# Kernel tuning notes

Hardware: AMD Instinct MI355X
Metric: run time of the kernel (lower is better)

Reference implementation:

```python
import jax, jax.numpy as jnp
import numpy as np

N = 100000   # nodes
E = 1600000  # edges
F_IN = 256   # input features
H = 64       # hidden
C = 40       # classes


def setup_inputs() -> dict:
    key = jax.random.key(0)
    k = jax.random.split(key, 5)
    x = jax.random.normal(k[0], (N, F_IN), dtype=jnp.float32)
    edge_index = jax.random.randint(k[1], (2, E), 0, N, dtype=jnp.int64)
    edge_attr = jax.random.uniform(k[2], (E,), dtype=jnp.float32)
    # GCNConv params (glorot-ish scale), biases zero like reset_parameters
    W1 = jax.random.normal(k[3], (F_IN, H), dtype=jnp.float32) * (1.0 / np.sqrt(F_IN))
    b1 = jnp.zeros((H,), dtype=jnp.float32)
    W2 = jax.random.normal(k[4], (H, C), dtype=jnp.float32) * (1.0 / np.sqrt(H))
    b2 = jnp.zeros((C,), dtype=jnp.float32)
    return {"x": x, "edge_index": edge_index, "edge_attr": edge_attr,
            "W1": W1, "b1": b1, "W2": W2, "b2": b2}


def _gcn_conv(x, W, b, src, dst, norm):
    h = x @ W                                   # [N, out]
    msg = h[src] * norm[:, None]                # gather + edge scale [E+N, out]
    out = jax.ops.segment_sum(msg, dst, num_segments=N)
    return out + b


def reference(x, edge_index, edge_attr, W1, b1, W2, b2):
    # gcn_norm: add self-loops (weight 1), symmetric D^-1/2 A D^-1/2
    loop = jnp.arange(N, dtype=edge_index.dtype)
    src = jnp.concatenate([edge_index[0], loop])
    dst = jnp.concatenate([edge_index[1], loop])
    w = jnp.concatenate([edge_attr, jnp.ones((N,), dtype=edge_attr.dtype)])
    deg = jax.ops.segment_sum(w, dst, num_segments=N)
    dinv = jnp.where(deg > 0, jax.lax.rsqrt(jnp.maximum(deg, 1e-30)), 0.0)
    norm = dinv[src] * w * dinv[dst]

    h = _gcn_conv(x, W1, b1, src, dst, norm)
    h = jax.nn.relu(h)                          # dropout is identity in eval mode
    h = _gcn_conv(h, W2, b2, src, dst, norm)
    return jax.nn.log_softmax(h, axis=1)
```

## Files before the change

kernel.cpp:

```cpp
#include <hip/hip_runtime.h>
#include <math.h>

#define NN   100000
#define NE   1600000
#define FIN  256
#define HID  64
#define NC   40
#define NBKT 391
#define EPB  6250
#define CAP  4608

typedef __attribute__((ext_vector_type(8))) short short8;
typedef __attribute__((ext_vector_type(4))) float float4v;

static __device__ __forceinline__ short f2bf(float f) {
    unsigned u = __float_as_uint(f);
    u += 0x7FFFu + ((u >> 16) & 1u);
    return (short)(u >> 16);
}
static __device__ __forceinline__ float bf2f(unsigned short b) {
    return __uint_as_float((unsigned)b << 16);
}

__global__ __launch_bounds__(256) void w1cvt_k(const float* __restrict__ W1,
                                               short* __restrict__ w1t) {
    int t = blockIdx.x * 256 + threadIdx.x;
    int k = t >> 6, n = t & 63;
    w1t[n * FIN + k] = f2bf(W1[k * HID + n]);
}

__global__ __launch_bounds__(256) void phaseA_k(const int* __restrict__ src,
                                                const int* __restrict__ dst,
                                                const float* __restrict__ w,
                                                int* __restrict__ cursor,
                                                int2* __restrict__ bucketbuf) {
    __shared__ int  hist[NBKT];
    __shared__ int  sc[512];
    __shared__ int  loc_base[NBKT];
    __shared__ int  loc_cur[NBKT];
    __shared__ int  gb[NBKT];
    __shared__ int2 buf[EPB];
    const int t  = threadIdx.x;
    const int e0 = blockIdx.x * EPB;

    for (int i = t; i < NBKT; i += 256) hist[i] = 0;
    __syncthreads();
    for (int i = t; i < EPB; i += 256) atomicAdd(&hist[dst[e0 + i] >> 8], 1);
    __syncthreads();
    sc[t]       = (t       < NBKT) ? hist[t]       : 0;
    sc[t + 256] = (t + 256 < NBKT) ? hist[t + 256] : 0;
    __syncthreads();
    for (int off = 1; off < 512; off <<= 1) {
        int a0 = (t >= off) ? sc[t - off] : 0;
        int a1 = sc[t + 256 - off];
        __syncthreads();
        sc[t] += a0; sc[t + 256] += a1;
        __syncthreads();
    }
    for (int i = t; i < NBKT; i += 256) {
        int base = sc[i] - hist[i];
        loc_base[i] = base;
        loc_cur[i]  = base;
        gb[i] = atomicAdd(&cursor[i * 16], hist[i]);
    }
    __syncthreads();
    for (int i = t; i < EPB; i += 256) {
        int e = e0 + i;
        int d = dst[e];
        int b = d >> 8;
        int p = atomicAdd(&loc_cur[b], 1);
        buf[p] = make_int2(src[e] | ((d & 255) << 17), __float_as_int(w[e]));
    }
    __syncthreads();
    for (int b = t; b < NBKT; b += 256) {
        int lb = loc_base[b], n = hist[b];
        int2* dstp = bucketbuf + (size_t)b * CAP + gb[b];
        for (int i = 0; i < n; ++i) dstp[i] = buf[lb + i];
    }
}

__global__ __launch_bounds__(512) void scanB_k(const int* __restrict__ cursor,
                                               int* __restrict__ bucketbase,
                                               int* __restrict__ row_start) {
    __shared__ int tmp[512];
    int t = threadIdx.x;
    int v = (t < NBKT) ? cursor[t * 16] : 0;
    tmp[t] = v;
    __syncthreads();
    for (int off = 1; off < 512; off <<= 1) {
        int add = (t >= off) ? tmp[t - off] : 0;
        __syncthreads(); tmp[t] += add; __syncthreads();
    }
    if (t < NBKT) bucketbase[t] = tmp[t] - v;
    if (t == 0) { bucketbase[NBKT] = NE; row_start[NN] = NE; }
}

__global__ __launch_bounds__(256) void phaseB_k(const int* __restrict__ bucketbase,
                                                const int2* __restrict__ bucketbuf,
                                                int2* __restrict__ e8,
                                                int* __restrict__ row_start,
                                                float* __restrict__ dinv) {
    __shared__ int2 buf[CAP];
    __shared__ int2 buf2[CAP];
    __shared__ int  hist2[256];
    __shared__ int  tmp[256];
    __shared__ int  base2[257];
    __shared__ int  cur2[256];
    const int b = blockIdx.x, t = threadIdx.x;
    const int g0   = bucketbase[b];
    const int cntb = bucketbase[b + 1] - g0;
    const int n0   = b * 256;
    const int nnb  = (NN - n0 < 256) ? (NN - n0) : 256;

    hist2[t] = 0;
    __syncthreads();
    const int2* bb = bucketbuf + (size_t)b * CAP;
    for (int i = t; i < cntb; i += 256) {
        int2 kv = bb[i];
        buf[i] = kv;
        atomicAdd(&hist2[kv.x >> 17], 1);
    }
    __syncthreads();
    int v = hist2[t];
    tmp[t] = v;
    __syncthreads();
    for (int off = 1; off < 256; off <<= 1) {
        int add = (t >= off) ? tmp[t - off] : 0;
        __syncthreads(); tmp[t] += add; __syncthreads();
    }
    int excl = tmp[t] - v;
    base2[t] = excl;
    cur2[t]  = excl;
    if (t == 0) base2[256] = cntb;
    if (t < nnb) row_start[n0 + t] = g0 + excl;
    __syncthreads();
    for (int i = t; i < cntb; i += 256) {
        int2 kv = buf[i];
        int d = kv.x >> 17;
        int p = atomicAdd(&cur2[d], 1);
        buf2[p] = make_int2(kv.x & 0x1FFFF, kv.y);
    }
    __syncthreads();
    for (int i = t; i < cntb; i += 256) e8[g0 + i] = buf2[i];
    if (t < nnb) {
        float s = 0.f;
        int j1 = base2[t + 1];
        for (int j = base2[t]; j < j1; ++j) s += __int_as_float(buf2[j].y);
        dinv[n0 + t] = rsqrtf(1.0f + s);
    }
}

__global__ __launch_bounds__(256) void gemm1_mfma_k(const float* __restrict__ x,
                                                    const short* __restrict__ w1t,
                                                    const float* __restrict__ dinv,
                                                    unsigned short* __restrict__ h1) {
    const int wave = threadIdx.x >> 6;
    const int lane = threadIdx.x & 63;
    const int m    = lane & 15;
    const int quad = lane >> 4;
    const int r0   = blockIdx.x * 64 + wave * 16;
    const int row  = r0 + m;
    const int rcl  = (row < NN) ? row : (NN - 1);
    const float* xrow = x + (size_t)rcl * FIN + quad * 8;

    float4v acc0 = {0.f,0.f,0.f,0.f}, acc1 = acc0, acc2 = acc0, acc3 = acc0;

#pragma unroll
    for (int kc = 0; kc < 8; ++kc) {
        const int kof = kc * 32 + quad * 8;
        float4 xa = *(const float4*)(xrow + kc * 32);
        float4 xb = *(const float4*)(xrow + kc * 32 + 4);
        short8 a;
        a[0] = f2bf(xa.x); a[1] = f2bf(xa.y); a[2] = f2bf(xa.z); a[3] = f2bf(xa.w);
        a[4] = f2bf(xb.x); a[5] = f2bf(xb.y); a[6] = f2bf(xb.z); a[7] = f2bf(xb.w);
        short8 b0 = *(const short8*)(w1t + (0 * 16 + m) * FIN + kof);
        short8 b1 = *(const short8*)(w1t + (1 * 16 + m) * FIN + kof);
        short8 b2 = *(const short8*)(w1t + (2 * 16 + m) * FIN + kof);
        short8 b3 = *(const short8*)(w1t + (3 * 16 + m) * FIN + kof);
        acc0 = __builtin_amdgcn_mfma_f32_16x16x32_bf16(a, b0, acc0, 0, 0, 0);
        acc1 = __builtin_amdgcn_mfma_f32_16x16x32_bf16(a, b1, acc1, 0, 0, 0);
        acc2 = __builtin_amdgcn_mfma_f32_16x16x32_bf16(a, b2, acc2, 0, 0, 0);
        acc3 = __builtin_amdgcn_mfma_f32_16x16x32_bf16(a, b3, acc3, 0, 0, 0);
    }
#pragma unroll
    for (int r = 0; r < 4; ++r) {
        int rr = r0 + quad * 4 + r;
        if (rr < NN) {
            float dv = dinv[rr];
            unsigned short* hp = h1 + (size_t)rr * HID + m;
            hp[0]  = (unsigned short)f2bf(acc0[r] * dv);
            hp[16] = (unsigned short)f2bf(acc1[r] * dv);
            hp[32] = (unsigned short)f2bf(acc2[r] * dv);
            hp[48] = (unsigned short)f2bf(acc3[r] * dv);
        }
    }
}

__global__ __launch_bounds__(256) void gatherA_k(const int* __restrict__ row_start,
                                                 const int2* __restrict__ e8,
                                                 const float* __restrict__ dinv,
                                                 const unsigned short* __restrict__ h,
                                                 const float* __restrict__ b1,
                                                 unsigned short* __restrict__ Rp) {
    const int v    = blockIdx.x * 4 + (threadIdx.x >> 6);
    const int lane = threadIdx.x & 63;
    const int half = lane >> 5;
    const int fp2  = (lane & 31) << 1;
    const int i0 = row_start[v], i1 = row_start[v + 1];

    float a0 = 0.f, a1 = 0.f, c0 = 0.f, c1 = 0.f;
    int i = i0 + half;
    for (; i + 2 < i1; i += 4) {
        int2 ea = e8[i];
        int2 eb = e8[i + 2];
        unsigned pa = *(const unsigned*)(h + (size_t)ea.x * HID + fp2);
        unsigned pb = *(const unsigned*)(h + (size_t)eb.x * HID + fp2);
        float wa = __int_as_float(ea.y), wb = __int_as_float(eb.y);
        a0 = fmaf(__uint_as_float(pa << 16),          wa, a0);
        a1 = fmaf(__uint_as_float(pa & 0xFFFF0000u), wa, a1);
        c0 = fmaf(__uint_as_float(pb << 16),          wb, c0);
        c1 = fmaf(__uint_as_float(pb & 0xFFFF0000u), wb, c1);
    }
    if (i < i1) {
        int2 ea = e8[i];
        unsigned pa = *(const unsigned*)(h + (size_t)ea.x * HID + fp2);
        float wa = __int_as_float(ea.y);
        a0 = fmaf(__uint_as_float(pa << 16),          wa, a0);
        a1 = fmaf(__uint_as_float(pa & 0xFFFF0000u), wa, a1);
    }
    a0 += c0; a1 += c1;
    a0 += __shfl_xor(a0, 32);
    a1 += __shfl_xor(a1, 32);

    const float dv = dinv[v];
    unsigned ps = *(const unsigned*)(h + (size_t)v * HID + fp2);
    float r0 = dv * (a0 + __uint_as_float(ps << 16));
    float r1 = dv * (a1 + __uint_as_float(ps & 0xFFFF0000u));
    r0 = fmaxf(r0 + b1[fp2],     0.f);
    r1 = fmaxf(r1 + b1[fp2 + 1], 0.f);
    if (half == 0) {
        unsigned pk = (unsigned)(unsigned short)f2bf(dv * r0)
                    | ((unsigned)(unsigned short)f2bf(dv * r1) << 16);
        *(unsigned*)(Rp + (size_t)v * HID + fp2) = pk;
    }
}

__global__ __launch_bounds__(256) void gatherB_k(const int* __restrict__ row_start,
                                                 const int2* __restrict__ e8,
                                                 const float* __restrict__ dinv,
                                                 const unsigned short* __restrict__ Rp,
                                                 float* __restrict__ agg2) {
    const int v    = blockIdx.x * 4 + (threadIdx.x >> 6);
    const int lane = threadIdx.x & 63;
    const int half = lane >> 5;
    const int fp2  = (lane & 31) << 1;
    const int i0 = row_start[v], i1 = row_start[v + 1];

    float a0 = 0.f, a1 = 0.f, c0 = 0.f, c1 = 0.f;
    int i = i0 + half;
    for (; i + 2 < i1; i += 4) {
        int2 ea = e8[i];
        int2 eb = e8[i + 2];
        unsigned pa = *(const unsigned*)(Rp + (size_t)ea.x * HID + fp2);
        unsigned pb = *(const unsigned*)(Rp + (size_t)eb.x * HID + fp2);
        float wa = __int_as_float(ea.y), wb = __int_as_float(eb.y);
        a0 = fmaf(__uint_as_float(pa << 16),          wa, a0);
        a1 = fmaf(__uint_as_float(pa & 0xFFFF0000u), wa, a1);
        c0 = fmaf(__uint_as_float(pb << 16),          wb, c0);
        c1 = fmaf(__uint_as_float(pb & 0xFFFF0000u), wb, c1);
    }
    if (i < i1) {
        int2 ea = e8[i];
        unsigned pa = *(const unsigned*)(Rp + (size_t)ea.x * HID + fp2);
        float wa = __int_as_float(ea.y);
        a0 = fmaf(__uint_as_float(pa << 16),          wa, a0);
        a1 = fmaf(__uint_as_float(pa & 0xFFFF0000u), wa, a1);
    }
    a0 += c0; a1 += c1;
    a0 += __shfl_xor(a0, 32);
    a1 += __shfl_xor(a1, 32);

    const float dv = dinv[v];
    unsigned ps = *(const unsigned*)(Rp + (size_t)v * HID + fp2);
    float r0 = dv * (a0 + __uint_as_float(ps << 16));
    float r1 = dv * (a1 + __uint_as_float(ps & 0xFFFF0000u));
    if (half == 0)
        *(float2*)(agg2 + (size_t)v * HID + fp2) = make_float2(r0, r1);
}

__global__ __launch_bounds__(256) void gemm3_logsm_k(const float* __restrict__ agg2,
                                                     const float* __restrict__ W2,
                                                     const float* __restrict__ b2,
                                                     float* __restrict__ out) {
    __shared__ float w2s[HID * NC];
    __shared__ float b2s[NC];
    for (int i = threadIdx.x; i < HID * NC; i += 256) w2s[i] = W2[i];
    if (threadIdx.x < NC) b2s[threadIdx.x] = b2[threadIdx.x];
    __syncthreads();

    const int r = blockIdx.x * 256 + threadIdx.x;
    if (r >= NN) return;
    float acc[NC];
#pragma unroll
    for (int c = 0; c < NC; ++c) acc[c] = b2s[c];

    const float4* row4 = (const float4*)(agg2 + (size_t)r * HID);
    for (int kk = 0; kk < HID; kk += 4) {
        float4 v = row4[kk >> 2];
#pragma unroll
        for (int c = 0; c < NC; ++c) {
            acc[c] = fmaf(v.x, w2s[(kk + 0) * NC + c], acc[c]);
            acc[c] = fmaf(v.y, w2s[(kk + 1) * NC + c], acc[c]);
            acc[c] = fmaf(v.z, w2s[(kk + 2) * NC + c], acc[c]);
            acc[c] = fmaf(v.w, w2s[(kk + 3) * NC + c], acc[c]);
        }
    }
    float m = acc[0];
#pragma unroll
    for (int c = 1; c < NC; ++c) m = fmaxf(m, acc[c]);
    float s = 0.f;
#pragma unroll
    for (int c = 0; c < NC; ++c) s += __expf(acc[c] - m);
    float lg = m + __logf(s);
    float* outp = out + (size_t)r * NC;
#pragma unroll
    for (int c = 0; c < NC; c += 4)
        *(float4*)&outp[c] = make_float4(acc[c] - lg, acc[c+1] - lg, acc[c+2] - lg, acc[c+3] - lg);
}

extern "C" void kernel_launch(void* const* d_in, const int* in_sizes, int n_in,
                              void* d_out, int out_size, void* d_ws, size_t ws_size,
                              hipStream_t stream) {
    const float* x  = (const float*)d_in[0];
    const int*   ei = (const int*)d_in[1];
    const float* ea = (const float*)d_in[2];
    const float* W1 = (const float*)d_in[3];
    const float* b1 = (const float*)d_in[4];
    const float* W2 = (const float*)d_in[5];
    const float* b2 = (const float*)d_in[6];
    const int* src = ei;
    const int* dst = ei + NE;
    float* out = (float*)d_out;

    char* ws = (char*)d_ws;
    float* dinv       = (float*)(ws + 0);
    int*   row_start  = (int*)  (ws + 400000);
    int*   cursor     = (int*)  (ws + 800016);
    int*   bucketbase = (int*)  (ws + 825040);
    int2*  e8         = (int2*) (ws + 826608);
    unsigned short* h1 = (unsigned short*)(ws + 13626608);
    unsigned short* Rp = (unsigned short*)(ws + 26426608);
    float* agg2       = (float*)(ws + 39226608);
    short* w1t        = (short*)(ws + 64826608);
    int2*  bucketbuf  = (int2*)agg2;

    hipMemsetAsync(cursor, 0, 391 * 16 * sizeof(int), stream);

    w1cvt_k <<<64,   256, 0, stream>>>(W1, w1t);
    phaseA_k<<<256,  256, 0, stream>>>(src, dst, ea, cursor, bucketbuf);
    scanB_k <<<1,    512, 0, stream>>>(cursor, bucketbase, row_start);
    phaseB_k<<<NBKT, 256, 0, stream>>>(bucketbase, bucketbuf, e8, row_start, dinv);

    gemm1_mfma_k <<<(NN + 63) / 64, 256, 0, stream>>>(x, w1t, dinv, h1);
    gatherA_k    <<<NN / 4, 256, 0, stream>>>(row_start, e8, dinv, h1, b1, Rp);
    gatherB_k    <<<NN / 4, 256, 0, stream>>>(row_start, e8, dinv, Rp, agg2);
    gemm3_logsm_k<<<(NN + 255) / 256, 256, 0, stream>>>(agg2, W2, b2, out);
}
```

Baseline: 412.1 us.

## Slice hidden features into four 16-wide planes for cache-resident gathers

Stores h1, Rp and agg2 as four feature-sliced planes of 16 columns each, so each plane of bf16 data (about 3.2 MB) can stay in cache. Each gather kernel now runs four times, once per slice, with 8 lanes per feature slice and 8 edge groups per wave, reduced with extra shuffles. The aim is to cut random-gather DRAM traffic through better L2/MALL locality, at the cost of reading the edge list four times per layer and launching eight gather kernels instead of two.

```diff
diff --git a/kernel.cpp b/kernel.cpp
--- a/kernel.cpp
+++ b/kernel.cpp
@@ -9,6 +9,7 @@
 #define NBKT 391
 #define EPB  6250
 #define CAP  4608
+#define SL   ((size_t)NN * 16)
 
 typedef __attribute__((ext_vector_type(8))) short short8;
 typedef __attribute__((ext_vector_type(4))) float float4v;
@@ -187,34 +188,36 @@
         int rr = r0 + quad * 4 + r;
         if (rr < NN) {
             float dv = dinv[rr];
-            unsigned short* hp = h1 + (size_t)rr * HID + m;
-            hp[0]  = (unsigned short)f2bf(acc0[r] * dv);
-            hp[16] = (unsigned short)f2bf(acc1[r] * dv);
-            hp[32] = (unsigned short)f2bf(acc2[r] * dv);
-            hp[48] = (unsigned short)f2bf(acc3[r] * dv);
+            size_t ro = (size_t)rr * 16 + m;
+            h1[ro]          = (unsigned short)f2bf(acc0[r] * dv);
+            h1[SL + ro]     = (unsigned short)f2bf(acc1[r] * dv);
+            h1[2 * SL + ro] = (unsigned short)f2bf(acc2[r] * dv);
+            h1[3 * SL + ro] = (unsigned short)f2bf(acc3[r] * dv);
         }
     }
 }
 
-__global__ __launch_bounds__(256) void gatherA_k(const int* __restrict__ row_start,
-                                                 const int2* __restrict__ e8,
-                                                 const float* __restrict__ dinv,
-                                                 const unsigned short* __restrict__ h,
-                                                 const float* __restrict__ b1,
-                                                 unsigned short* __restrict__ Rp) {
+__global__ __launch_bounds__(256) void gatherAs_k(const int* __restrict__ row_start,
+                                                  const int2* __restrict__ e8,
+                                                  const float* __restrict__ dinv,
+                                                  const unsigned short* __restrict__ h1,
+                                                  const float* __restrict__ b1,
+                                                  unsigned short* __restrict__ Rp,
+                                                  int s) {
     const int v    = blockIdx.x * 4 + (threadIdx.x >> 6);
     const int lane = threadIdx.x & 63;
-    const int half = lane >> 5;
-    const int fp2  = (lane & 31) << 1;
+    const int eg   = lane >> 3;
+    const int f    = lane & 7;
+    const unsigned short* hs = h1 + (size_t)s * SL;
     const int i0 = row_start[v], i1 = row_start[v + 1];
 
     float a0 = 0.f, a1 = 0.f, c0 = 0.f, c1 = 0.f;
-    int i = i0 + half;
-    for (; i + 2 < i1; i += 4) {
+    int i = i0 + eg;
+    for (; i + 8 < i1; i += 16) {
         int2 ea = e8[i];
-        int2 eb = e8[i + 2];
-        unsigned pa = *(const unsigned*)(h + (size_t)ea.x * HID + fp2);
-        unsigned pb = *(const unsigned*)(h + (size_t)eb.x * HID + fp2);
+        int2 eb = e8[i + 8];
+        unsigned pa = *(const unsigned*)(hs + (size_t)ea.x * 16 + f * 2);
+        unsigned pb = *(const unsigned*)(hs + (size_t)eb.x * 16 + f * 2);
         float wa = __int_as_float(ea.y), wb = __int_as_float(eb.y);
         a0 = fmaf(__uint_as_float(pa << 16),          wa, a0);
         a1 = fmaf(__uint_as_float(pa & 0xFFFF0000u), wa, a1);
@@ -223,46 +226,50 @@
     }
     if (i < i1) {
         int2 ea = e8[i];
-        unsigned pa = *(const unsigned*)(h + (size_t)ea.x * HID + fp2);
+        unsigned pa = *(const unsigned*)(hs + (size_t)ea.x * 16 + f * 2);
         float wa = __int_as_float(ea.y);
         a0 = fmaf(__uint_as_float(pa << 16),          wa, a0);
         a1 = fmaf(__uint_as_float(pa & 0xFFFF0000u), wa, a1);
     }
     a0 += c0; a1 += c1;
-    a0 += __shfl_xor(a0, 32);
-    a1 += __shfl_xor(a1, 32);
+    a0 += __shfl_xor(a0, 8);  a1 += __shfl_xor(a1, 8);
+    a0 += __shfl_xor(a0, 16); a1 += __shfl_xor(a1, 16);
+    a0 += __shfl_xor(a0, 32); a1 += __shfl_xor(a1, 32);
 
     const float dv = dinv[v];
-    unsigned ps = *(const unsigned*)(h + (size_t)v * HID + fp2);
+    unsigned ps = *(const unsigned*)(hs + (size_t)v * 16 + f * 2);
     float r0 = dv * (a0 + __uint_as_float(ps << 16));
     float r1 = dv * (a1 + __uint_as_float(ps & 0xFFFF0000u));
-    r0 = fmaxf(r0 + b1[fp2],     0.f);
-    r1 = fmaxf(r1 + b1[fp2 + 1], 0.f);
-    if (half == 0) {
+    float2 bb = *(const float2*)(b1 + s * 16 + f * 2);
+    r0 = fmaxf(r0 + bb.x, 0.f);
+    r1 = fmaxf(r1 + bb.y, 0.f);
+    if (eg == 0) {
         unsigned pk = (unsigned)(unsigned short)f2bf(dv * r0)
                     | ((unsigned)(unsigned short)f2bf(dv * r1) << 16);
-        *(unsigned*)(Rp + (size_t)v * HID + fp2) = pk;
-    }
-}
-
-__global__ __launch_bounds__(256) void gatherB_k(const int* __restrict__ row_start,
-                                                 const int2* __restrict__ e8,
-                                                 const float* __restrict__ dinv,
-                                                 const unsigned short* __restrict__ Rp,
-                                                 float* __restrict__ agg2) {
+        *(unsigned*)(Rp + (size_t)s * SL + (size_t)v * 16 + f * 2) = pk;
+    }
+}
+
+__global__ __launch_bounds__(256) void gatherBs_k(const int* __restrict__ row_start,
+                                                  const int2* __restrict__ e8,
+                                                  const float* __restrict__ dinv,
+                                                  const unsigned short* __restrict__ Rp,
+                                                  float* __restrict__ agg2,
+                                                  int s) {
     const int v    = blockIdx.x * 4 + (threadIdx.x >> 6);
     const int lane = threadIdx.x & 63;
-    const int half = lane >> 5;
-    const int fp2  = (lane & 31) << 1;
+    const int eg   = lane >> 3;
+    const int f    = lane & 7;
+    const unsigned short* hs = Rp + (size_t)s * SL;
     const int i0 = row_start[v], i1 = row_start[v + 1];
 
     float a0 = 0.f, a1 = 0.f, c0 = 0.f, c1 = 0.f;
-    int i = i0 + half;
-    for (; i + 2 < i1; i += 4) {
+    int i = i0 + eg;
+    for (; i + 8 < i1; i += 16) {
         int2 ea = e8[i];
-        int2 eb = e8[i + 2];
-        unsigned pa = *(const unsigned*)(Rp + (size_t)ea.x * HID + fp2);
-        unsigned pb = *(const unsigned*)(Rp + (size_t)eb.x * HID + fp2);
+        int2 eb = e8[i + 8];
+        unsigned pa = *(const unsigned*)(hs + (size_t)ea.x * 16 + f * 2);
+        unsigned pb = *(const unsigned*)(hs + (size_t)eb.x * 16 + f * 2);
         float wa = __int_as_float(ea.y), wb = __int_as_float(eb.y);
         a0 = fmaf(__uint_as_float(pa << 16),          wa, a0);
         a1 = fmaf(__uint_as_float(pa & 0xFFFF0000u), wa, a1);
@@ -271,21 +278,22 @@
     }
     if (i < i1) {
         int2 ea = e8[i];
-        unsigned pa = *(const unsigned*)(Rp + (size_t)ea.x * HID + fp2);
+        unsigned pa = *(const unsigned*)(hs + (size_t)ea.x * 16 + f * 2);
         float wa = __int_as_float(ea.y);
         a0 = fmaf(__uint_as_float(pa << 16),          wa, a0);
         a1 = fmaf(__uint_as_float(pa & 0xFFFF0000u), wa, a1);
     }
     a0 += c0; a1 += c1;
-    a0 += __shfl_xor(a0, 32);
-    a1 += __shfl_xor(a1, 32);
+    a0 += __shfl_xor(a0, 8);  a1 += __shfl_xor(a1, 8);
+    a0 += __shfl_xor(a0, 16); a1 += __shfl_xor(a1, 16);
+    a0 += __shfl_xor(a0, 32); a1 += __shfl_xor(a1, 32);
 
     const float dv = dinv[v];
-    unsigned ps = *(const unsigned*)(Rp + (size_t)v * HID + fp2);
+    unsigned ps = *(const unsigned*)(hs + (size_t)v * 16 + f * 2);
     float r0 = dv * (a0 + __uint_as_float(ps << 16));
     float r1 = dv * (a1 + __uint_as_float(ps & 0xFFFF0000u));
-    if (half == 0)
-        *(float2*)(agg2 + (size_t)v * HID + fp2) = make_float2(r0, r1);
+    if (eg == 0)
+        *(float2*)(agg2 + (size_t)s * SL + (size_t)v * 16 + f * 2) = make_float2(r0, r1);
 }
 
 __global__ __launch_bounds__(256) void gemm3_logsm_k(const float* __restrict__ agg2,
@@ -304,15 +312,20 @@
 #pragma unroll
     for (int c = 0; c < NC; ++c) acc[c] = b2s[c];
 
-    const float4* row4 = (const float4*)(agg2 + (size_t)r * HID);
-    for (int kk = 0; kk < HID; kk += 4) {
-        float4 v = row4[kk >> 2];
-#pragma unroll
-        for (int c = 0; c < NC; ++c) {
-            acc[c] = fmaf(v.x, w2s[(kk + 0) * NC + c], acc[c]);
-            acc[c] = fmaf(v.y, w2s[(kk + 1) * NC + c], acc[c]);
-            acc[c] = fmaf(v.z, w2s[(kk + 2) * NC + c], acc[c]);
-            acc[c] = fmaf(v.w, w2s[(kk + 3) * NC + c], acc[c]);
+#pragma unroll
+    for (int s = 0; s < 4; ++s) {
+        const float* base = agg2 + (size_t)s * SL + (size_t)r * 16;
+#pragma unroll
+        for (int q = 0; q < 4; ++q) {
+            float4 v = *(const float4*)(base + q * 4);
+            const int kk = s * 16 + q * 4;
+#pragma unroll
+            for (int c = 0; c < NC; ++c) {
+                acc[c] = fmaf(v.x, w2s[(kk + 0) * NC + c], acc[c]);
+                acc[c] = fmaf(v.y, w2s[(kk + 1) * NC + c], acc[c]);
+                acc[c] = fmaf(v.z, w2s[(kk + 2) * NC + c], acc[c]);
+                acc[c] = fmaf(v.w, w2s[(kk + 3) * NC + c], acc[c]);
+            }
         }
     }
     float m = acc[0];
@@ -362,7 +375,9 @@
     phaseB_k<<<NBKT, 256, 0, stream>>>(bucketbase, bucketbuf, e8, row_start, dinv);
 
     gemm1_mfma_k <<<(NN + 63) / 64, 256, 0, stream>>>(x, w1t, dinv, h1);
-    gatherA_k    <<<NN / 4, 256, 0, stream>>>(row_start, e8, dinv, h1, b1, Rp);
-    gatherB_k    <<<NN / 4, 256, 0, stream>>>(row_start, e8, dinv, Rp, agg2);
+    for (int s = 0; s < 4; ++s)
+        gatherAs_k<<<NN / 4, 256, 0, stream>>>(row_start, e8, dinv, h1, b1, Rp, s);
+    for (int s = 0; s < 4; ++s)
+        gatherBs_k<<<NN / 4, 256, 0, stream>>>(row_start, e8, dinv, Rp, agg2, s);
     gemm3_logsm_k<<<(NN + 255) / 256, 256, 0, stream>>>(agg2, W2, b2, out);
 }
```

New measurement: 544.2 us. 32.1% more time.
